# Optimization experiments

Hardware: AMD Instinct MI355X
Metric: run time of the kernel (lower is better)

The kernel has to match this reference:

```python
import jax, jax.numpy as jnp
import numpy as np

SIGMA = 1.0
KSIZE = 5
WEAK = 75.0
STRONG = 255.0
LOW_T = 0.00392
HIGH_T = 0.15

# scipy.signal.gaussian(M, std): unnormalized gaussian window
_n = np.arange(KSIZE, dtype=np.float32) - (KSIZE - 1) / 2.0
_g = np.exp(-0.5 * (_n / SIGMA) ** 2).astype(np.float32)
GAUSS_H = jnp.asarray(_g.reshape(1, 1, 1, KSIZE))  # horizontal 1xK
GAUSS_V = jnp.asarray(_g.reshape(1, 1, KSIZE, 1))  # vertical Kx1

_sobel = np.array([[1, 0, -1], [2, 0, -2], [1, 0, -1]], dtype=np.float32)
SOBEL_H = jnp.asarray(_sobel.reshape(1, 1, 3, 3))
SOBEL_V = jnp.asarray(_sobel.T.reshape(1, 1, 3, 3))

_f0 = np.array([[0, 0, 0], [0, 1, -1], [0, 0, 0]], np.float32)
_f45 = np.array([[0, 0, 0], [0, 1, 0], [0, 0, -1]], np.float32)
_f90 = np.array([[0, 0, 0], [0, 1, 0], [0, -1, 0]], np.float32)
_f135 = np.array([[0, 0, 0], [0, 1, 0], [-1, 0, 0]], np.float32)
_f180 = np.array([[0, 0, 0], [-1, 1, 0], [0, 0, 0]], np.float32)
_f225 = np.array([[-1, 0, 0], [0, 1, 0], [0, 0, 0]], np.float32)
_f270 = np.array([[0, -1, 0], [0, 1, 0], [0, 0, 0]], np.float32)
_f315 = np.array([[0, 0, -1], [0, 1, 0], [0, 0, 0]], np.float32)
DIR_FILT = jnp.asarray(np.stack([_f0, _f45, _f90, _f135, _f180, _f225, _f270, _f315]).reshape(8, 1, 3, 3))

NBR_FILT = jnp.asarray(np.array([[1, 1, 1], [1, 0, 1], [1, 1, 1]], np.float32).reshape(1, 1, 3, 3))


def _conv(x, w, pad):
    # cross-correlation, matching torch F.conv2d
    return jax.lax.conv_general_dilated(
        x, w, window_strides=(1, 1), padding=[(pad[0], pad[0]), (pad[1], pad[1])],
        dimension_numbers=('NCHW', 'OIHW', 'NCHW'))


def setup_inputs() -> dict:
    key = jax.random.key(0)
    img = jax.random.uniform(key, (16, 1, 1024, 1024), dtype=jnp.float32)
    return {"img": img}


def reference(img):
    B = img.shape[0]
    # --- gaussian noise removal (separable) ---
    sm = _conv(img, GAUSS_H, (0, KSIZE // 2))
    sm = _conv(sm, GAUSS_V, (KSIZE // 2, 0))
    # --- sobel gradients ---
    Ix = _conv(sm, SOBEL_H, (1, 1))
    Iy = _conv(sm, SOBEL_V, (1, 1))
    mag = jnp.sqrt(Ix ** 2 + Iy ** 2)
    mag = mag / mag.reshape(B, -1).max(axis=1).reshape(B, 1, 1, 1)
    direction = jnp.arctan2(Iy, Ix) * (180.0 / 3.1415926) + 180.0
    direction = jnp.round(direction / 45.0) * 45.0
    # --- non-max suppression via directional differences + gather ---
    all_filtered = _conv(mag, DIR_FILT, (1, 1))  # [B,8,H,W]
    idx_pos = (direction / 45.0).astype(jnp.int32) % 8  # [B,1,H,W]
    idx_neg = (idx_pos + 4) % 8
    cs_pos = jnp.take_along_axis(all_filtered, idx_pos, axis=1)
    cs_neg = jnp.take_along_axis(all_filtered, idx_neg, axis=1)
    is_max = jnp.minimum(cs_pos, cs_neg) > 0.0
    thin = jnp.where(is_max, mag, 0.0)
    # --- double threshold ---
    hi = thin.max() * HIGH_T  # global max, as in source
    strong = thin >= hi
    weak = (thin < hi) & (thin >= LOW_T)
    inter = jnp.where(strong, STRONG, jnp.where(weak, WEAK, 0.0))
    # --- hysteresis: iterate until no weak pixel gains a strong neighbor ---
    def cond(state):
        return state[1]

    def body(state):
        x, _ = state
        weak_m = x == WEAK
        sn = _conv((x == STRONG).astype(jnp.float32), NBR_FILT, (1, 1))
        new_strong = weak_m & (sn > 0.0)
        x = jnp.where(new_strong, STRONG, x)
        return x, new_strong.any()

    final, _ = jax.lax.while_loop(cond, body, (inter, jnp.asarray(True)))
    final = jnp.where(final == STRONG, final, 0.0)
    return final
```

## Files before the change

### kernel.cpp

```cpp
#include <hip/hip_runtime.h>
#include <math.h>

#define BB 16
#define H 1024
#define W 1024
#define HW (H*W)
#define NTOT (BB*HW)

typedef unsigned long long u64;

__device__ __constant__ float GW[5] = {
    0.13533528323661270f, 0.60653065971263342f, 1.0f,
    0.60653065971263342f, 0.13533528323661270f};

__device__ __constant__ int NBDY[8] = {0, 1, 1, 1, 0, -1, -1, -1};
__device__ __constant__ int NBDX[8] = {1, 1, 0, -1, -1, -1, 0, 1};

#define CSCALE ((float)(180.0 / 3.1415926))

__device__ __forceinline__ float atan_poly01(float xin) {
    float y0 = 0.0f, x = xin;
    if (xin > 0.41421356f) {
        x = __fdividef(xin - 1.0f, xin + 1.0f);
        y0 = 0.78539816339f;
    }
    float z = x * x;
    float p = ((8.05374449538e-2f * z - 1.38776856032e-1f) * z + 1.99777106478e-1f) * z
              - 3.33329491539e-1f;
    return y0 + (p * z * x + x);
}

#define TW 128
#define TH 16
__global__ __launch_bounds__(256, 6) void k_smooth_sobel(const float* __restrict__ img,
                                                         float* __restrict__ mag,
                                                         unsigned char* __restrict__ bucket,
                                                         float* __restrict__ partial) {
#pragma clang fp contract(off)
    __shared__ float sA[22 * 136];
    __shared__ float sB[22 * 132];
    __shared__ float red[256];

    const int tid = threadIdx.x;
    const int x0 = blockIdx.x * TW;
    const int y0 = blockIdx.y * TH;
    const int b = blockIdx.z;
    const size_t base = (size_t)b * HW;

    for (int idx = tid; idx < 22 * 34; idx += 256) {
        int r = idx / 34, v = idx % 34;
        int gy = y0 - 3 + r;
        int gxv = x0 - 4 + v * 4;
        float4 val = make_float4(0.f, 0.f, 0.f, 0.f);
        if (gy >= 0 && gy < H && gxv >= 0 && gxv <= W - 4)
            val = *(const float4*)&img[base + (size_t)gy * W + gxv];
        *(float4*)&sA[r * 136 + v * 4] = val;
    }
    __syncthreads();

    for (int idx = tid; idx < 22 * 130; idx += 256) {
        int r = idx / 130, c = idx % 130;
        const float* row = &sA[r * 136 + c + 1];
        float s = 0.0f;
#pragma unroll
        for (int k = 0; k < 5; ++k) s = s + GW[k] * row[k];
        sB[r * 132 + c] = s;
    }
    __syncthreads();

    for (int idx = tid; idx < 18 * 130; idx += 256) {
        int rr = idx / 130, c = idx % 130;
        float s = 0.0f;
#pragma unroll
        for (int k = 0; k < 5; ++k) s = s + GW[k] * sB[(rr + k) * 132 + c];
        sA[rr * 136 + c] = s;
    }
    __syncthreads();

    float tmax = 0.0f;
#pragma unroll
    for (int k2 = 0; k2 < 2; ++k2) {
        int v = tid + k2 * 256;
        int r = v >> 5;
        int cg4 = (v & 31) * 4;
        int y = y0 + r;
        const bool ym = (y > 0), yp = (y < H - 1);

        float mg[4];
        unsigned int bk = 0;
#pragma unroll
        for (int j = 0; j < 4; ++j) {
            int c = cg4 + j;
            int x = x0 + c;
            const bool xm = (x > 0), xp = (x < W - 1);

            float a00 = 0.f, a01 = 0.f, a02 = 0.f, a10 = 0.f, a12 = 0.f,
                  a20 = 0.f, a21 = 0.f, a22 = 0.f;
            if (ym) {
                if (xm) a00 = sA[r * 136 + c];
                a01 = sA[r * 136 + c + 1];
                if (xp) a02 = sA[r * 136 + c + 2];
            }
            if (xm) a10 = sA[(r + 1) * 136 + c];
            if (xp) a12 = sA[(r + 1) * 136 + c + 2];
            if (yp) {
                if (xm) a20 = sA[(r + 2) * 136 + c];
                a21 = sA[(r + 2) * 136 + c + 1];
                if (xp) a22 = sA[(r + 2) * 136 + c + 2];
            }

            float Ix = a00;
            Ix = Ix - a02;
            Ix = Ix + 2.0f * a10;
            Ix = Ix - 2.0f * a12;
            Ix = Ix + a20;
            Ix = Ix - a22;

            float Iy = a00;
            Iy = Iy + 2.0f * a01;
            Iy = Iy + a02;
            Iy = Iy - a20;
            Iy = Iy - 2.0f * a21;
            Iy = Iy - a22;

            float t1 = Ix * Ix;
            float t2 = Iy * Iy;
            float m = sqrtf(t1 + t2);
            mg[j] = m;
            tmax = fmaxf(tmax, m);

            float ax = fabsf(Ix), ay = fabsf(Iy);
            float mn = fminf(ax, ay), mx = fmaxf(ax, ay);
            float zr = __fdividef(mn, mx);
            float bse = atan_poly01(zr);
            float phi = (ay > ax) ? (1.57079632679f - bse) : bse;
            if (Ix < 0.0f) phi = 3.14159265359f - phi;
            float theta = (Iy >= 0.0f) ? phi : -phi;
            float t = (theta * CSCALE + 180.0f) * (1.0f / 45.0f);
            float rr2 = rintf(t);
            if ((mx < 1e-30f) || (0.5f - fabsf(t - rr2) < 1e-4f)) {
                float fa2 = (float)atan2((double)Iy, (double)Ix);
                float d2 = fa2 * CSCALE;
                d2 = d2 + 180.0f;
                float t2d = d2 / 45.0f;
                rr2 = rintf(t2d);
            }
            int bidx = ((int)rr2) % 8;
            bk |= ((unsigned int)bidx) << (8 * j);
        }
        *(float4*)&mag[base + (size_t)y * W + x0 + cg4] = make_float4(mg[0], mg[1], mg[2], mg[3]);
        *(unsigned int*)&bucket[base + (size_t)y * W + x0 + cg4] = bk;
    }

    red[tid] = tmax;
    __syncthreads();
    for (int s = 128; s > 0; s >>= 1) {
        if (tid < s) red[tid] = fmaxf(red[tid], red[tid + s]);
        __syncthreads();
    }
    if (tid == 0) {
        int pb = (blockIdx.z * 64 + blockIdx.y) * 8 + blockIdx.x;
        partial[pb] = red[0];
    }
}

__global__ __launch_bounds__(256) void k_redmax_img(const float* __restrict__ partial,
                                                    float* __restrict__ magmax) {
    __shared__ float red[256];
    const float* p = partial + blockIdx.x * 512;
    float m = fmaxf(p[threadIdx.x], p[threadIdx.x + 256]);
    red[threadIdx.x] = m;
    __syncthreads();
    for (int s = 128; s > 0; s >>= 1) {
        if (threadIdx.x < s) red[threadIdx.x] = fmaxf(red[threadIdx.x], red[threadIdx.x + s]);
        __syncthreads();
    }
    if (threadIdx.x == 0) magmax[blockIdx.x] = red[0];
}

__global__ __launch_bounds__(1024) void k_redmax_all(const float* __restrict__ partial,
                                                     float* __restrict__ thinmax) {
    __shared__ float red[1024];
    float m = 0.0f;
    for (int k = threadIdx.x; k < 4096; k += 1024) m = fmaxf(m, partial[k]);
    red[threadIdx.x] = m;
    __syncthreads();
    for (int s = 512; s > 0; s >>= 1) {
        if (threadIdx.x < s) red[threadIdx.x] = fmaxf(red[threadIdx.x], red[threadIdx.x + s]);
        __syncthreads();
    }
    if (threadIdx.x == 0) *thinmax = red[0];
}

__global__ __launch_bounds__(256, 8) void k_nms_t(const float* __restrict__ mag,
                                                  const unsigned char* __restrict__ bucket,
                                                  const float* __restrict__ magmax,
                                                  float* __restrict__ thin,
                                                  float* __restrict__ partial) {
#pragma clang fp contract(off)
    __shared__ float sN[34 * 136];
    __shared__ float red[256];

    const int tid = threadIdx.x;
    const int x0 = blockIdx.x * 128;
    const int y0 = blockIdx.y * 32;
    const int b = blockIdx.z;
    const size_t base = (size_t)b * HW;
    const float M = magmax[b];

    for (int idx = tid; idx < 34 * 34; idx += 256) {
        int r = idx / 34, v = idx % 34;
        int gy = y0 - 1 + r;
        int gxv = x0 - 4 + v * 4;
        float4 val = make_float4(0.f, 0.f, 0.f, 0.f);
        if (gy >= 0 && gy < H && gxv >= 0 && gxv <= W - 4)
            val = *(const float4*)&mag[base + (size_t)gy * W + gxv];
        val.x = val.x / M;
        val.y = val.y / M;
        val.z = val.z / M;
        val.w = val.w / M;
        *(float4*)&sN[r * 136 + v * 4] = val;
    }
    __syncthreads();

    float tmax = 0.0f;
#pragma unroll
    for (int k4 = 0; k4 < 4; ++k4) {
        int v = tid + k4 * 256;
        int r = v >> 5;
        int cg4 = (v & 31) * 4;
        int y = y0 + r;

        unsigned int bk = *(const unsigned int*)&bucket[base + (size_t)y * W + x0 + cg4];
        float tv[4];
#pragma unroll
        for (int j = 0; j < 4; ++j) {
            int c = cg4 + j;
            int idx = (bk >> (8 * j)) & 0xff;
            int dy = NBDY[idx], dx = NBDX[idx];
            float mp = sN[(r + 1) * 136 + c + 4];
            float npv = sN[(r + 1 + dy) * 136 + c + 4 + dx];
            float nnv = sN[(r + 1 - dy) * 136 + c + 4 - dx];
            float cs_p = mp - npv;
            float cs_n = mp - nnv;
            tv[j] = (fminf(cs_p, cs_n) > 0.0f) ? mp : 0.0f;
            tmax = fmaxf(tmax, tv[j]);
        }
        *(float4*)&thin[base + (size_t)y * W + x0 + cg4] = make_float4(tv[0], tv[1], tv[2], tv[3]);
    }

    red[tid] = tmax;
    __syncthreads();
    for (int s = 128; s > 0; s >>= 1) {
        if (tid < s) red[tid] = fmaxf(red[tid], red[tid + s]);
        __syncthreads();
    }
    if (tid == 0) {
        int pb = (blockIdx.z * 32 + blockIdx.y) * 8 + blockIdx.x;
        partial[pb] = red[0];
    }
}

__global__ __launch_bounds__(256) void k_thresh4(const float* __restrict__ thin,
                                                 const float* __restrict__ thinmax,
                                                 u64* __restrict__ Sb,
                                                 u64* __restrict__ Wb) {
#pragma clang fp contract(off)
    const int tid = threadIdx.x;
    const int b = blockIdx.x >> 10;
    const int y = blockIdx.x & (H - 1);
    const float hi = (*thinmax) * 0.15f;

    const float4 t4 = *(const float4*)&thin[(size_t)blockIdx.x * 1024 + tid * 4];
    float tvals[4] = {t4.x, t4.y, t4.z, t4.w};
    unsigned int nibS = 0, nibW = 0;
#pragma unroll
    for (int j = 0; j < 4; ++j) {
        bool strong = (tvals[j] >= hi);
        bool weak = (!strong) && (tvals[j] >= 0.00392f);
        nibS |= (strong ? 1u : 0u) << j;
        nibW |= (weak ? 1u : 0u) << j;
    }
    __shared__ unsigned char ns[256], nw[256];
    ns[tid] = (unsigned char)nibS;
    nw[tid] = (unsigned char)nibW;
    __syncthreads();

    if (tid < 16) {
        u64 sw = 0, ww = 0;
#pragma unroll
        for (int j = 0; j < 16; ++j) {
            sw |= (u64)ns[tid * 16 + j] << (4 * j);
            ww |= (u64)nw[tid * 16 + j] << (4 * j);
        }
        const int ty = y >> 6, row = y & 63;
        const int widx = ((b << 8) | (ty << 4) | tid) * 64 + row;
        Sb[widx] = sw;
        Wb[widx] = ww;
    }
}

__global__ __launch_bounds__(256) void k_hyster_bits(const u64* __restrict__ Wb,
                                                     u64* __restrict__ Sb) {
    const int lane = threadIdx.x & 63;
    const int t = blockIdx.x * 4 + (threadIdx.x >> 6);
    const int ty = (t >> 4) & 15;
    const int tx = t & 15;
    const int idx = t * 64 + lane;

    u64 S = Sb[idx];
    const u64 Wk = Wb[idx];

    u64 hstat = 0;
    if (tx > 0)  hstat |= (Sb[(t - 1) * 64 + lane] >> 63) & 1ull;
    if (tx < 15) hstat |= (Sb[(t + 1) * 64 + lane] & 1ull) << 63;

    u64 halo = 0;
    if (lane == 0 && ty > 0) {
        const int ta = t - 16;
        u64 tc = Sb[ta * 64 + 63];
        u64 hh = (tc << 1) | tc | (tc >> 1);
        if (tx > 0)  hh |= (Sb[(ta - 1) * 64 + 63] >> 63) & 1ull;
        if (tx < 15) hh |= (Sb[(ta + 1) * 64 + 63] & 1ull) << 63;
        halo = hh;
    }
    if (lane == 63 && ty < 15) {
        const int tb = t + 16;
        u64 tc = Sb[tb * 64 + 0];
        u64 hh = (tc << 1) | tc | (tc >> 1);
        if (tx > 0)  hh |= (Sb[(tb - 1) * 64 + 0] >> 63) & 1ull;
        if (tx < 15) hh |= (Sb[(tb + 1) * 64 + 0] & 1ull) << 63;
        halo = hh;
    }

    for (int it = 0; it < 160; ++it) {
        u64 h = (S << 1) | S | (S >> 1) | hstat;
        u64 up = __shfl_up(h, 1, 64);
        if (lane == 0) up = halo;
        u64 dn = __shfl_down(h, 1, 64);
        if (lane == 63) dn = halo;
        u64 dil = h | up | dn;
        u64 nS = S | (Wk & dil);
        bool ch = (nS != S);
        S = nS;
        if (!__any(ch)) break;
    }

    Sb[idx] = S;
}

__global__ __launch_bounds__(256) void k_final4(const u64* __restrict__ Sb,
                                                float* __restrict__ out) {
    const int gid = blockIdx.x * 256 + threadIdx.x;
    const int p0 = gid * 4;
    const int x = p0 & (W - 1);
    const int y = (p0 >> 10) & (H - 1);
    const int b = p0 >> 20;
    const int widx = ((b << 8) | ((y >> 6) << 4) | (x >> 6)) * 64 + (y & 63);
    const u64 w = Sb[widx];
    const unsigned int nib = (unsigned int)((w >> (x & 63)) & 0xFull);
    float4 o;
    o.x = (nib & 1u) ? 255.0f : 0.0f;
    o.y = (nib & 2u) ? 255.0f : 0.0f;
    o.z = (nib & 4u) ? 255.0f : 0.0f;
    o.w = (nib & 8u) ? 255.0f : 0.0f;
    *(float4*)&out[p0] = o;
}

extern "C" void kernel_launch(void* const* d_in, const int* in_sizes, int n_in,
                              void* d_out, int out_size, void* d_ws, size_t ws_size,
                              hipStream_t stream) {
    (void)in_sizes; (void)n_in; (void)out_size; (void)ws_size;
    const float* img = (const float*)d_in[0];
    float* out = (float*)d_out;

    float* hdr = (float*)d_ws;
    float* partialA = (float*)((char*)d_ws + 256);
    float* partialB = partialA + 8192;
    float* A = partialB + 4096;
    unsigned char* C = (unsigned char*)(A + (size_t)NTOT);
    u64* Sb = (u64*)(C + (size_t)NTOT);
    u64* Wb = Sb + NTOT / 64;

    dim3 blk(256);
    k_smooth_sobel<<<dim3(W / TW, H / TH, BB), blk, 0, stream>>>(img, A, C, partialA);
    k_redmax_img<<<dim3(BB), blk, 0, stream>>>(partialA, hdr);
    k_nms_t<<<dim3(8, 32, BB), blk, 0, stream>>>(A, C, hdr, out, partialB);
    k_redmax_all<<<dim3(1), dim3(1024), 0, stream>>>(partialB, hdr + 16);
    k_thresh4<<<dim3(NTOT / 1024), blk, 0, stream>>>(out, hdr + 16, Sb, Wb);
    for (int p = 0; p < 6; ++p)
        k_hyster_bits<<<dim3(NTOT / (64 * 64) / 4), blk, 0, stream>>>(Wb, Sb);
    k_final4<<<dim3(NTOT / 1024), blk, 0, stream>>>(Sb, out);
}
```

Before: 264.6 us.

## Emit NMS result as bitmask, threshold on raw magnitude via bisected cutoffs

```diff
diff --git a/kernel.cpp b/kernel.cpp
--- a/kernel.cpp
+++ b/kernel.cpp
@@ -37,7 +37,7 @@
                                                          unsigned char* __restrict__ bucket,
                                                          float* __restrict__ partial) {
 #pragma clang fp contract(off)
-    __shared__ float sA[22 * 136];
+    __shared__ float sA[22 * 136 + 16];
     __shared__ float sB[22 * 132];
     __shared__ float red[256];
 
@@ -48,7 +48,7 @@
     const size_t base = (size_t)b * HW;
 
     for (int idx = tid; idx < 22 * 34; idx += 256) {
-        int r = idx / 34, v = idx % 34;
+        int r = idx / 34, v = idx - r * 34;
         int gy = y0 - 3 + r;
         int gxv = x0 - 4 + v * 4;
         float4 val = make_float4(0.f, 0.f, 0.f, 0.f);
@@ -58,22 +58,47 @@
     }
     __syncthreads();
 
-    for (int idx = tid; idx < 22 * 130; idx += 256) {
-        int r = idx / 130, c = idx % 130;
-        const float* row = &sA[r * 136 + c + 1];
-        float s = 0.0f;
-#pragma unroll
-        for (int k = 0; k < 5; ++k) s = s + GW[k] * row[k];
-        sB[r * 132 + c] = s;
-    }
-    __syncthreads();
-
-    for (int idx = tid; idx < 18 * 130; idx += 256) {
-        int rr = idx / 130, c = idx % 130;
-        float s = 0.0f;
-#pragma unroll
-        for (int k = 0; k < 5; ++k) s = s + GW[k] * sB[(rr + k) * 132 + c];
-        sA[rr * 136 + c] = s;
+    for (int idx = tid; idx < 22 * 33; idx += 256) {
+        int r = idx / 33, g = idx - r * 33;
+        const float* p = &sA[r * 136 + g * 4];
+        float4 A0 = *(const float4*)p;
+        float4 A1 = *(const float4*)(p + 4);
+        float4 A2 = *(const float4*)(p + 8);
+        float a_[12] = {A0.x, A0.y, A0.z, A0.w, A1.x, A1.y, A1.z, A1.w,
+                        A2.x, A2.y, A2.z, A2.w};
+        float o[4];
+#pragma unroll
+        for (int j = 0; j < 4; ++j) {
+            float s = 0.0f;
+#pragma unroll
+            for (int k = 0; k < 5; ++k) s = s + GW[k] * a_[j + 1 + k];
+            o[j] = s;
+        }
+        *(float4*)&sB[r * 132 + g * 4] = make_float4(o[0], o[1], o[2], o[3]);
+    }
+    __syncthreads();
+
+    for (int idx = tid; idx < 18 * 33; idx += 256) {
+        int rr = idx / 33, g = idx - rr * 33;
+        float bb[20];
+#pragma unroll
+        for (int k = 0; k < 5; ++k) {
+            float4 t = *(const float4*)&sB[(rr + k) * 132 + g * 4];
+            bb[k * 4 + 0] = t.x; bb[k * 4 + 1] = t.y;
+            bb[k * 4 + 2] = t.z; bb[k * 4 + 3] = t.w;
+        }
+        int gy = y0 - 1 + rr;
+        bool rowok = (gy >= 0 && gy < H);
+        float o[4];
+#pragma unroll
+        for (int j = 0; j < 4; ++j) {
+            float s = 0.0f;
+#pragma unroll
+            for (int k = 0; k < 5; ++k) s = s + GW[k] * bb[k * 4 + j];
+            int gx = x0 - 1 + g * 4 + j;
+            o[j] = (rowok && gx >= 0 && gx < W) ? s : 0.0f;
+        }
+        *(float4*)&sA[rr * 136 + g * 4] = make_float4(o[0], o[1], o[2], o[3]);
     }
     __syncthreads();
 
@@ -82,32 +107,25 @@
     for (int k2 = 0; k2 < 2; ++k2) {
         int v = tid + k2 * 256;
         int r = v >> 5;
-        int cg4 = (v & 31) * 4;
+        int cg = (v & 31) * 4;
         int y = y0 + r;
-        const bool ym = (y > 0), yp = (y < H - 1);
+        const float* P0 = &sA[r * 136 + cg];
+        const float* P1 = P0 + 136;
+        const float* P2 = P1 + 136;
+        float4 q0 = *(const float4*)P0; float2 e0 = *(const float2*)(P0 + 4);
+        float4 q1 = *(const float4*)P1; float2 e1 = *(const float2*)(P1 + 4);
+        float4 q2 = *(const float4*)P2; float2 e2 = *(const float2*)(P2 + 4);
+        float r0[6] = {q0.x, q0.y, q0.z, q0.w, e0.x, e0.y};
+        float r1[6] = {q1.x, q1.y, q1.z, q1.w, e1.x, e1.y};
+        float r2[6] = {q2.x, q2.y, q2.z, q2.w, e2.x, e2.y};
 
         float mg[4];
         unsigned int bk = 0;
 #pragma unroll
         for (int j = 0; j < 4; ++j) {
-            int c = cg4 + j;
-            int x = x0 + c;
-            const bool xm = (x > 0), xp = (x < W - 1);
-
-            float a00 = 0.f, a01 = 0.f, a02 = 0.f, a10 = 0.f, a12 = 0.f,
-                  a20 = 0.f, a21 = 0.f, a22 = 0.f;
-            if (ym) {
-                if (xm) a00 = sA[r * 136 + c];
-                a01 = sA[r * 136 + c + 1];
-                if (xp) a02 = sA[r * 136 + c + 2];
-            }
-            if (xm) a10 = sA[(r + 1) * 136 + c];
-            if (xp) a12 = sA[(r + 1) * 136 + c + 2];
-            if (yp) {
-                if (xm) a20 = sA[(r + 2) * 136 + c];
-                a21 = sA[(r + 2) * 136 + c + 1];
-                if (xp) a22 = sA[(r + 2) * 136 + c + 2];
-            }
+            float a00 = r0[j], a01 = r0[j + 1], a02 = r0[j + 2];
+            float a10 = r1[j],                  a12 = r1[j + 2];
+            float a20 = r2[j], a21 = r2[j + 1], a22 = r2[j + 2];
 
             float Ix = a00;
             Ix = Ix - a02;
@@ -145,11 +163,11 @@
                 float t2d = d2 / 45.0f;
                 rr2 = rintf(t2d);
             }
-            int bidx = ((int)rr2) % 8;
+            int bidx = ((int)rr2) & 7;
             bk |= ((unsigned int)bidx) << (8 * j);
         }
-        *(float4*)&mag[base + (size_t)y * W + x0 + cg4] = make_float4(mg[0], mg[1], mg[2], mg[3]);
-        *(unsigned int*)&bucket[base + (size_t)y * W + x0 + cg4] = bk;
+        *(float4*)&mag[base + (size_t)y * W + x0 + cg] = make_float4(mg[0], mg[1], mg[2], mg[3]);
+        *(unsigned int*)&bucket[base + (size_t)y * W + x0 + cg] = bk;
     }
 
     red[tid] = tmax;
@@ -192,10 +210,10 @@
     if (threadIdx.x == 0) *thinmax = red[0];
 }
 
-__global__ __launch_bounds__(256, 8) void k_nms_t(const float* __restrict__ mag,
+__global__ __launch_bounds__(256, 8) void k_nms_b(const float* __restrict__ mag,
                                                   const unsigned char* __restrict__ bucket,
                                                   const float* __restrict__ magmax,
-                                                  float* __restrict__ thin,
+                                                  u64* __restrict__ Mb,
                                                   float* __restrict__ partial) {
 #pragma clang fp contract(off)
     __shared__ float sN[34 * 136];
@@ -209,94 +227,104 @@
     const float M = magmax[b];
 
     for (int idx = tid; idx < 34 * 34; idx += 256) {
-        int r = idx / 34, v = idx % 34;
+        int r = idx / 34, v = idx - r * 34;
         int gy = y0 - 1 + r;
         int gxv = x0 - 4 + v * 4;
         float4 val = make_float4(0.f, 0.f, 0.f, 0.f);
         if (gy >= 0 && gy < H && gxv >= 0 && gxv <= W - 4)
             val = *(const float4*)&mag[base + (size_t)gy * W + gxv];
-        val.x = val.x / M;
-        val.y = val.y / M;
-        val.z = val.z / M;
-        val.w = val.w / M;
         *(float4*)&sN[r * 136 + v * 4] = val;
     }
     __syncthreads();
 
-    float tmax = 0.0f;
-#pragma unroll
-    for (int k4 = 0; k4 < 4; ++k4) {
-        int v = tid + k4 * 256;
-        int r = v >> 5;
-        int cg4 = (v & 31) * 4;
+    const int wv = tid >> 6, L = tid & 63;
+    const int h = wv & 1, wr = wv >> 1;
+    const int txw = (x0 >> 6) + h;
+    float amax = 0.0f;
+
+#pragma unroll
+    for (int i = 0; i < 16; ++i) {
+        int r = i * 2 + wr;
+        int c = h * 64 + L;
         int y = y0 + r;
-
-        unsigned int bk = *(const unsigned int*)&bucket[base + (size_t)y * W + x0 + cg4];
-        float tv[4];
-#pragma unroll
-        for (int j = 0; j < 4; ++j) {
-            int c = cg4 + j;
-            int idx = (bk >> (8 * j)) & 0xff;
-            int dy = NBDY[idx], dx = NBDX[idx];
-            float mp = sN[(r + 1) * 136 + c + 4];
-            float npv = sN[(r + 1 + dy) * 136 + c + 4 + dx];
-            float nnv = sN[(r + 1 - dy) * 136 + c + 4 - dx];
-            float cs_p = mp - npv;
-            float cs_n = mp - nnv;
-            tv[j] = (fminf(cs_p, cs_n) > 0.0f) ? mp : 0.0f;
-            tmax = fmaxf(tmax, tv[j]);
-        }
-        *(float4*)&thin[base + (size_t)y * W + x0 + cg4] = make_float4(tv[0], tv[1], tv[2], tv[3]);
-    }
-
-    red[tid] = tmax;
+        unsigned int bkt = bucket[base + (size_t)y * W + x0 + c];
+        int dy = NBDY[bkt], dx = NBDX[bkt];
+        float a  = sN[(r + 1) * 136 + c + 4];
+        float bp = sN[(r + 1 + dy) * 136 + c + 4 + dx];
+        float bn = sN[(r + 1 - dy) * 136 + c + 4 - dx];
+        bool g1 = a > bp, g2 = a > bn;
+        bool f1 = a >= bp * 1.0000005f;
+        bool f2 = a >= bn * 1.0000005f;
+        bool r1 = g1, r2 = g2;
+        if (__any((g1 && !f1) || (g2 && !f2))) {
+            float qa = a / M;
+            if (g1 && !f1) r1 = qa > (bp / M);
+            if (g2 && !f2) r2 = qa > (bn / M);
+        }
+        bool im = r1 && r2;
+        if (im) amax = fmaxf(amax, a);
+        u64 word = __ballot(im);
+        if (L == 0) {
+            int ty = y >> 6, row = y & 63;
+            Mb[((b << 8) | (ty << 4) | txw) * 64 + row] = word;
+        }
+    }
+
+    red[tid] = amax;
     __syncthreads();
     for (int s = 128; s > 0; s >>= 1) {
         if (tid < s) red[tid] = fmaxf(red[tid], red[tid + s]);
         __syncthreads();
     }
-    if (tid == 0) {
-        int pb = (blockIdx.z * 32 + blockIdx.y) * 8 + blockIdx.x;
-        partial[pb] = red[0];
-    }
-}
-
-__global__ __launch_bounds__(256) void k_thresh4(const float* __restrict__ thin,
-                                                 const float* __restrict__ thinmax,
-                                                 u64* __restrict__ Sb,
-                                                 u64* __restrict__ Wb) {
-#pragma clang fp contract(off)
+    if (tid == 0)
+        partial[(blockIdx.z * 32 + blockIdx.y) * 8 + blockIdx.x] = red[0] / M;
+}
+
+__global__ void k_bisect(const float* __restrict__ hdr, float* __restrict__ thr) {
+    int t = threadIdx.x;
+    if (t >= 32) return;
+    int b = t >> 1;
+    float M = hdr[b];
+    float T = (t & 1) ? (hdr[16] * 0.15f) : 0.00392f;
+    if (0.0f / M >= T) { thr[t] = 0.0f; return; }
+    unsigned int lo = 0u, hi = 0x7f800000u;
+    while (hi - lo > 1u) {
+        unsigned int mid = lo + ((hi - lo) >> 1);
+        if (__uint_as_float(mid) / M >= T) hi = mid; else lo = mid;
+    }
+    thr[t] = __uint_as_float(hi);
+}
+
+__global__ __launch_bounds__(256) void k_thresh_b(const float* __restrict__ mag,
+                                                  const u64* __restrict__ Mb,
+                                                  const float* __restrict__ hdr,
+                                                  const float* __restrict__ thr,
+                                                  u64* __restrict__ Sb,
+                                                  u64* __restrict__ Wb) {
     const int tid = threadIdx.x;
-    const int b = blockIdx.x >> 10;
-    const int y = blockIdx.x & (H - 1);
-    const float hi = (*thinmax) * 0.15f;
-
-    const float4 t4 = *(const float4*)&thin[(size_t)blockIdx.x * 1024 + tid * 4];
-    float tvals[4] = {t4.x, t4.y, t4.z, t4.w};
-    unsigned int nibS = 0, nibW = 0;
-#pragma unroll
-    for (int j = 0; j < 4; ++j) {
-        bool strong = (tvals[j] >= hi);
-        bool weak = (!strong) && (tvals[j] >= 0.00392f);
-        nibS |= (strong ? 1u : 0u) << j;
-        nibW |= (weak ? 1u : 0u) << j;
-    }
-    __shared__ unsigned char ns[256], nw[256];
-    ns[tid] = (unsigned char)nibS;
-    nw[tid] = (unsigned char)nibW;
-    __syncthreads();
-
-    if (tid < 16) {
-        u64 sw = 0, ww = 0;
-#pragma unroll
-        for (int j = 0; j < 16; ++j) {
-            sw |= (u64)ns[tid * 16 + j] << (4 * j);
-            ww |= (u64)nw[tid * 16 + j] << (4 * j);
-        }
-        const int ty = y >> 6, row = y & 63;
-        const int widx = ((b << 8) | (ty << 4) | tid) * 64 + row;
-        Sb[widx] = sw;
-        Wb[widx] = ww;
+    const int x0 = blockIdx.x * 128;
+    const int y0 = blockIdx.y * 32;
+    const int b = blockIdx.z;
+    const size_t base = (size_t)b * HW;
+    const float Alo = thr[b * 2], Ahi = thr[b * 2 + 1];
+    const bool snm = (hdr[16] * 0.15f <= 0.0f);
+    const int wv = tid >> 6, L = tid & 63;
+    const int h = wv & 1, wr = wv >> 1;
+    const int txw = (x0 >> 6) + h;
+
+#pragma unroll
+    for (int i = 0; i < 16; ++i) {
+        int r = i * 2 + wr;
+        int y = y0 + r;
+        float a = mag[base + (size_t)y * W + x0 + h * 64 + L];
+        int ty = y >> 6, row = y & 63;
+        int widx = ((b << 8) | (ty << 4) | txw) * 64 + row;
+        bool im = (Mb[widx] >> L) & 1ull;
+        bool strong = snm || (im && (a >= Ahi));
+        bool weak = (!strong) && im && (a >= Alo);
+        u64 sw = __ballot(strong);
+        u64 ww = __ballot(weak);
+        if (L == 0) { Sb[widx] = sw; Wb[widx] = ww; }
     }
 }
 
@@ -334,12 +362,12 @@
     }
 
     for (int it = 0; it < 160; ++it) {
-        u64 h = (S << 1) | S | (S >> 1) | hstat;
-        u64 up = __shfl_up(h, 1, 64);
+        u64 hh = (S << 1) | S | (S >> 1) | hstat;
+        u64 up = __shfl_up(hh, 1, 64);
         if (lane == 0) up = halo;
-        u64 dn = __shfl_down(h, 1, 64);
+        u64 dn = __shfl_down(hh, 1, 64);
         if (lane == 63) dn = halo;
-        u64 dil = h | up | dn;
+        u64 dil = hh | up | dn;
         u64 nS = S | (Wk & dil);
         bool ch = (nS != S);
         S = nS;
@@ -375,19 +403,22 @@
     float* out = (float*)d_out;
 
     float* hdr = (float*)d_ws;
-    float* partialA = (float*)((char*)d_ws + 256);
+    float* thr = hdr + 64;
+    float* partialA = hdr + 128;
     float* partialB = partialA + 8192;
     float* A = partialB + 4096;
     unsigned char* C = (unsigned char*)(A + (size_t)NTOT);
     u64* Sb = (u64*)(C + (size_t)NTOT);
     u64* Wb = Sb + NTOT / 64;
+    u64* Mb = Wb + NTOT / 64;
 
     dim3 blk(256);
-    k_smooth_sobel<<<dim3(W / TW, H / TH, BB), blk, 0, stream>>>(img, A, C, partialA);
+    k_smooth_sobel<<<dim3(8, 64, BB), blk, 0, stream>>>(img, A, C, partialA);
     k_redmax_img<<<dim3(BB), blk, 0, stream>>>(partialA, hdr);
-    k_nms_t<<<dim3(8, 32, BB), blk, 0, stream>>>(A, C, hdr, out, partialB);
+    k_nms_b<<<dim3(8, 32, BB), blk, 0, stream>>>(A, C, hdr, Mb, partialB);
     k_redmax_all<<<dim3(1), dim3(1024), 0, stream>>>(partialB, hdr + 16);
-    k_thresh4<<<dim3(NTOT / 1024), blk, 0, stream>>>(out, hdr + 16, Sb, Wb);
+    k_bisect<<<dim3(1), dim3(64), 0, stream>>>(hdr, thr);
+    k_thresh_b<<<dim3(8, 32, BB), blk, 0, stream>>>(A, Mb, hdr, thr, Sb, Wb);
     for (int p = 0; p < 6; ++p)
         k_hyster_bits<<<dim3(NTOT / (64 * 64) / 4), blk, 0, stream>>>(Wb, Sb);
     k_final4<<<dim3(NTOT / 1024), blk, 0, stream>>>(Sb, out);
```

After: 268.1 us. About the same (+1.3%).
